# Kernel optimization log

Hardware: AMD Instinct MI355X
Metric: run time of the kernel (lower is better)

## Reference

```python
import jax, jax.numpy as jnp
import numpy as np

_K = 256  # d_model // 8


def setup_inputs() -> dict:
    key = jax.random.key(0)
    ks = jax.random.split(key, 7)
    B, T, D = 4, 4096, 2048
    x = jax.random.normal(ks[0], (B, T, D), jnp.float32)
    ema_mean = 0.1 * jax.random.normal(ks[1], (D,), jnp.float32)
    # ensure positive variance: ema_sq - ema_mean^2 in [0.5, 1.5]
    ema_sq = ema_mean ** 2 + 0.5 + jax.random.uniform(ks[2], (D,), jnp.float32)
    ema_out = jax.random.normal(ks[3], (D,), jnp.float32)
    log_tau = 0.1 * jax.random.normal(ks[4], (), jnp.float32)
    log_sigma_raw = 0.1 * jax.random.normal(ks[5], (), jnp.float32)
    log_w_raw = 0.1 * jax.random.normal(ks[6], (), jnp.float32)
    return {
        "x": x,
        "ema_mean": ema_mean,
        "ema_sq": ema_sq,
        "ema_out": ema_out,
        "log_tau": log_tau,
        "log_sigma_raw": log_sigma_raw,
        "log_w_raw": log_w_raw,
    }


def reference(x, ema_mean, ema_sq, ema_out, log_tau, log_sigma_raw, log_w_raw):
    tau = jnp.exp(log_tau)
    sigma = jax.nn.softplus(log_sigma_raw) + 0.01
    w = jax.nn.softplus(log_w_raw)

    out = jax.nn.gelu(x, approximate=False)  # F.gelu default = exact erf

    # z-score against EMA stats
    std = jnp.sqrt(jnp.clip(ema_sq - ema_mean ** 2, 1e-6, None))
    z = (x - ema_mean) / std

    # topk |z| over channel dim, gather z, mean of |z_topk|
    _, idx = jax.lax.top_k(jnp.abs(z), _K)          # idx: [B,T,K]
    z_topk = jnp.take_along_axis(z, idx, axis=-1)
    topk_mean = jnp.mean(jnp.abs(z_topk), axis=-1, keepdims=True)  # [B,T,1]
    surp = jnp.tanh(sigma * topk_mean)

    # cosine similarity of gelu output against EMA output direction
    ema_u = ema_out / (jnp.linalg.norm(ema_out) + 1e-8)
    out_n = out / jnp.maximum(
        jnp.linalg.norm(out, axis=-1, keepdims=True), 1e-12
    )  # F.normalize eps
    cos_out = jnp.sum(out_n * ema_u, axis=-1, keepdims=True)  # [B,T,1]

    gate = jnp.exp(-tau * cos_out) * (1.0 + w * surp)
    return out * gate
```

## Files before the change

kernel.cpp:

```cpp
#include <hip/hip_runtime.h>
#include <math.h>

#define D      2048
#define KSEL   256
#define NT     256
#define NBINS  512
#define ROWS   2

typedef float f4 __attribute__((ext_vector_type(4)));
typedef int   i4 __attribute__((ext_vector_type(4)));

__device__ __forceinline__ float fast_gelu(float x) {
    float x2 = x * x;
    float t  = fmaf(x2, -0.0713548162f, -1.5957691216f);
    float e  = __expf(x * t);
    return x * __builtin_amdgcn_rcpf(1.0f + e);
}

template<int CTRL, int RMASK>
__device__ __forceinline__ float dpp_mov_f(float v) {
    int r = __builtin_amdgcn_update_dpp(0, __builtin_bit_cast(int, v),
                                        CTRL, RMASK, 0xf, true);
    return __builtin_bit_cast(float, r);
}
template<int CTRL, int RMASK>
__device__ __forceinline__ int dpp_mov_i(int v) {
    return __builtin_amdgcn_update_dpp(0, v, CTRL, RMASK, 0xf, true);
}
__device__ __forceinline__ float wave_scan_f(float x) {
    x += dpp_mov_f<0x111, 0xf>(x);
    x += dpp_mov_f<0x112, 0xf>(x);
    x += dpp_mov_f<0x114, 0xf>(x);
    x += dpp_mov_f<0x118, 0xf>(x);
    x += dpp_mov_f<0x142, 0xa>(x);
    x += dpp_mov_f<0x143, 0xc>(x);
    return x;
}
__device__ __forceinline__ int wave_scan_i(int x) {
    x += dpp_mov_i<0x111, 0xf>(x);
    x += dpp_mov_i<0x112, 0xf>(x);
    x += dpp_mov_i<0x114, 0xf>(x);
    x += dpp_mov_i<0x118, 0xf>(x);
    x += dpp_mov_i<0x142, 0xa>(x);
    x += dpp_mov_i<0x143, 0xc>(x);
    return x;
}

__global__ __launch_bounds__(NT) void prep_kernel(
    const float* __restrict__ ema_mean,
    const float* __restrict__ ema_sq,
    const float* __restrict__ ema_out,
    const float* __restrict__ p_log_tau,
    const float* __restrict__ p_log_sigma,
    const float* __restrict__ p_log_w,
    float* __restrict__ ws)
{
    __shared__ float red[4];
    const int tid = threadIdx.x;
    float ss = 0.f;
#pragma unroll
    for (int k = 0; k < D / NT; ++k) {
        int i = tid + k * NT;
        float m = ema_mean[i];
        float v = fmaxf(fmaf(-m, m, ema_sq[i]), 1e-6f);
        float inv = 64.0f * __builtin_amdgcn_rsqf(v);
        ws[i]     = inv;
        ws[D + i] = -m * inv;
        float e = ema_out[i];
        ss = fmaf(e, e, ss);
    }
    ss = wave_scan_f(ss);
    if ((tid & 63) == 63) red[tid >> 6] = ss;
    __syncthreads();
    float inv_nrm = 1.0f / (sqrtf(red[0] + red[1] + red[2] + red[3]) + 1e-8f);
#pragma unroll
    for (int k = 0; k < D / NT; ++k) {
        int i = tid + k * NT;
        ws[2 * D + i] = ema_out[i] * inv_nrm;
    }
    if (tid == 0) {
        ws[3 * D + 0] = __expf(p_log_tau[0]);
        ws[3 * D + 1] = __logf(1.0f + __expf(p_log_sigma[0])) + 0.01f;
        ws[3 * D + 2] = __logf(1.0f + __expf(p_log_w[0]));
    }
}

__global__ __launch_bounds__(NT) void row_kernel(
    const float* __restrict__ x,
    const float* __restrict__ ws,
    float* __restrict__ out)
{
    __shared__ int   hist[NBINS];
    __shared__ float red[4][3];
    __shared__ int   bsel_sh, krem_sh;

    const int t    = threadIdx.x;
    const int wave = t >> 6;
    const int lane = t & 63;

    const float tau   = ws[3 * D + 0];
    const float sigma = ws[3 * D + 1];
    const float w     = ws[3 * D + 2];

    f4 aa = ((const f4*)ws)[t];
    f4 ab = ((const f4*)ws)[t + NT];
    f4 ba = ((const f4*)(ws + D))[t];
    f4 bb = ((const f4*)(ws + D))[t + NT];
    f4 ua = ((const f4*)(ws + 2 * D))[t];
    f4 ub = ((const f4*)(ws + 2 * D))[t + NT];
    const float a_[8] = {aa.x,aa.y,aa.z,aa.w, ab.x,ab.y,ab.z,ab.w};
    const float b_[8] = {ba.x,ba.y,ba.z,ba.w, bb.x,bb.y,bb.z,bb.w};
    const float u_[8] = {ua.x,ua.y,ua.z,ua.w, ub.x,ub.y,ub.z,ub.w};

    const size_t row0 = (size_t)blockIdx.x * ROWS;
    f4 xa = ((const f4*)(x + row0 * D))[t];
    f4 xb = ((const f4*)(x + row0 * D))[t + NT];

    hist[t] = 0;
    hist[t + NT] = 0;
    __syncthreads();

#pragma unroll
    for (int r = 0; r < ROWS; ++r) {
        const float xv[8] = {xa.x,xa.y,xa.z,xa.w, xb.x,xb.y,xb.z,xb.w};

        float g[8], av[8];
        float dot = 0.f, nrm = 0.f;
#pragma unroll
        for (int j = 0; j < 8; ++j) {
            float gg = fast_gelu(xv[j]);
            g[j] = gg;
            av[j] = fabsf(fmaf(xv[j], a_[j], b_[j]));
            dot = fmaf(gg, u_[j], dot);
            nrm = fmaf(gg, gg, nrm);
        }

        if (r + 1 < ROWS) {
            const float* xn = x + (row0 + r + 1) * D;
            xa = ((const f4*)xn)[t];
            xb = ((const f4*)xn)[t + NT];
        }

#pragma unroll
        for (int j = 0; j < 8; ++j) {
            int bin = (int)av[j];
            bin = bin > NBINS - 1 ? NBINS - 1 : bin;
            atomicAdd(&hist[(NBINS - 1) - bin], 1);
        }
        __syncthreads();

        if (wave == 0) {
            i4 va = *(const i4*)&hist[8 * lane];
            i4 vb = *(const i4*)&hist[8 * lane + 4];
            int c0 = va.x;
            int c1 = c0 + va.y;
            int c2 = c1 + va.z;
            int c3 = c2 + va.w;
            int c4 = c3 + vb.x;
            int c5 = c4 + vb.y;
            int c6 = c5 + vb.z;
            int c7 = c6 + vb.w;
            int incl = wave_scan_i(c7);
            int excl = incl - c7;
            int pre[8] = {0, c0, c1, c2, c3, c4, c5, c6};
            int cum[8] = {c0, c1, c2, c3, c4, c5, c6, c7};
#pragma unroll
            for (int k = 0; k < 8; ++k) {
                int s = excl + pre[k];
                int e = excl + cum[k];
                if (s < KSEL && e >= KSEL) {
                    bsel_sh = (NBINS - 1) - (8 * lane + k);
                    krem_sh = KSEL - s;
                }
            }
        }
        __syncthreads();

        const int   bsel = bsel_sh;
        const int   krem = krem_sh;
        const float hi  = (bsel == NBINS - 1) ? __builtin_inff() : (float)(bsel + 1);
        const float mid = (float)bsel + 0.5f;

        float s = 0.f;
#pragma unroll
        for (int j = 0; j < 8; ++j) {
            s += (av[j] >= hi) ? av[j] : 0.f;
        }

        dot = wave_scan_f(dot);
        nrm = wave_scan_f(nrm);
        s   = wave_scan_f(s);
        if (lane == 63) {
            red[wave][0] = dot; red[wave][1] = nrm; red[wave][2] = s;
        }
        hist[t] = 0;
        hist[t + NT] = 0;
        __syncthreads();

        dot = red[0][0] + red[1][0] + red[2][0] + red[3][0];
        nrm = red[0][1] + red[1][1] + red[2][1] + red[3][1];
        s   = red[0][2] + red[1][2] + red[2][2] + red[3][2];

        const float topk_mean = (s + (float)krem * mid) * (1.0f / (64.0f * KSEL));
        const float cosv = dot * __builtin_amdgcn_rsqf(fmaxf(nrm, 1e-24f));
        const float yt = sigma * topk_mean;
        const float et = __expf(-2.0f * yt);
        const float th = (1.0f - et) * __builtin_amdgcn_rcpf(1.0f + et);
        const float gate = __expf(-tau * cosv) * fmaf(w, th, 1.0f);

        f4 oa, ob;
        oa.x = g[0]*gate; oa.y = g[1]*gate; oa.z = g[2]*gate; oa.w = g[3]*gate;
        ob.x = g[4]*gate; ob.y = g[5]*gate; ob.z = g[6]*gate; ob.w = g[7]*gate;
        f4* outr = (f4*)(out + (row0 + r) * D);
        __builtin_nontemporal_store(oa, outr + t);
        __builtin_nontemporal_store(ob, outr + t + NT);
    }
}

extern "C" void kernel_launch(void* const* d_in, const int* in_sizes, int n_in,
                              void* d_out, int out_size, void* d_ws, size_t ws_size,
                              hipStream_t stream) {
    (void)n_in; (void)out_size; (void)ws_size;
    const float* x         = (const float*)d_in[0];
    const float* ema_mean  = (const float*)d_in[1];
    const float* ema_sq    = (const float*)d_in[2];
    const float* ema_out   = (const float*)d_in[3];
    const float* log_tau   = (const float*)d_in[4];
    const float* log_sigma = (const float*)d_in[5];
    const float* log_w     = (const float*)d_in[6];
    float* out = (float*)d_out;
    float* ws  = (float*)d_ws;

    prep_kernel<<<1, NT, 0, stream>>>(ema_mean, ema_sq, ema_out,
                                      log_tau, log_sigma, log_w, ws);
    const int rows = in_sizes[0] / D;
    row_kernel<<<rows / ROWS, NT, 0, stream>>>(x, ws, out);
}
```

Before: 50.20 us.

## Assign one row per wave with private histograms and fp16-packed register storage

The row kernel now maps one row to each wavefront instead of one row to the whole block. Each wave keeps its own LDS histogram and does its reductions with DPP scans plus readlane, so the block-wide __syncthreads barriers and the shared reduction buffers go away. To hold a whole row per lane (32 values), the GELU outputs and |z| values are stored packed as fp16, which reduces register pressure. The cost is lower precision: outputs are rounded through fp16 and top-k sums use fp16 |z| values. Each wave also reloads the EMA coefficient vectors itself, and the fp16 output error may exceed tolerance.

```diff
diff --git a/kernel.cpp b/kernel.cpp
--- a/kernel.cpp
+++ b/kernel.cpp
@@ -5,10 +5,11 @@
 #define KSEL   256
 #define NT     256
 #define NBINS  512
-#define ROWS   2
-
-typedef float f4 __attribute__((ext_vector_type(4)));
-typedef int   i4 __attribute__((ext_vector_type(4)));
+#define WPB    4
+
+typedef float  f4 __attribute__((ext_vector_type(4)));
+typedef int    i4 __attribute__((ext_vector_type(4)));
+typedef __fp16 h2 __attribute__((ext_vector_type(2)));
 
 __device__ __forceinline__ float fast_gelu(float x) {
     float x2 = x * x;
@@ -44,6 +45,20 @@
     x += dpp_mov_i<0x142, 0xa>(x);
     x += dpp_mov_i<0x143, 0xc>(x);
     return x;
+}
+__device__ __forceinline__ int wave_or_i(int x) {
+    x |= dpp_mov_i<0x111, 0xf>(x);
+    x |= dpp_mov_i<0x112, 0xf>(x);
+    x |= dpp_mov_i<0x114, 0xf>(x);
+    x |= dpp_mov_i<0x118, 0xf>(x);
+    x |= dpp_mov_i<0x142, 0xa>(x);
+    x |= dpp_mov_i<0x143, 0xc>(x);
+    return x;
+}
+__device__ __forceinline__ float wave_total_f(float x) {
+    float s = wave_scan_f(x);
+    int r = __builtin_amdgcn_readlane(__builtin_bit_cast(int, s), 63);
+    return __builtin_bit_cast(float, r);
 }
 
 __global__ __launch_bounds__(NT) void prep_kernel(
@@ -90,130 +105,129 @@
     const float* __restrict__ ws,
     float* __restrict__ out)
 {
-    __shared__ int   hist[NBINS];
-    __shared__ float red[4][3];
-    __shared__ int   bsel_sh, krem_sh;
+    __shared__ int hist[WPB * NBINS];
 
     const int t    = threadIdx.x;
-    const int wave = t >> 6;
+    const int wid  = t >> 6;
     const int lane = t & 63;
+    int* __restrict__ h = &hist[wid * NBINS];
+
+    *(i4*)&h[8 * lane]     = (i4)0;
+    *(i4*)&h[8 * lane + 4] = (i4)0;
 
     const float tau   = ws[3 * D + 0];
     const float sigma = ws[3 * D + 1];
     const float w     = ws[3 * D + 2];
 
-    f4 aa = ((const f4*)ws)[t];
-    f4 ab = ((const f4*)ws)[t + NT];
-    f4 ba = ((const f4*)(ws + D))[t];
-    f4 bb = ((const f4*)(ws + D))[t + NT];
-    f4 ua = ((const f4*)(ws + 2 * D))[t];
-    f4 ub = ((const f4*)(ws + 2 * D))[t + NT];
-    const float a_[8] = {aa.x,aa.y,aa.z,aa.w, ab.x,ab.y,ab.z,ab.w};
-    const float b_[8] = {ba.x,ba.y,ba.z,ba.w, bb.x,bb.y,bb.z,bb.w};
-    const float u_[8] = {ua.x,ua.y,ua.z,ua.w, ub.x,ub.y,ub.z,ub.w};
-
-    const size_t row0 = (size_t)blockIdx.x * ROWS;
-    f4 xa = ((const f4*)(x + row0 * D))[t];
-    f4 xb = ((const f4*)(x + row0 * D))[t + NT];
-
-    hist[t] = 0;
-    hist[t + NT] = 0;
-    __syncthreads();
-
-#pragma unroll
-    for (int r = 0; r < ROWS; ++r) {
-        const float xv[8] = {xa.x,xa.y,xa.z,xa.w, xb.x,xb.y,xb.z,xb.w};
-
-        float g[8], av[8];
-        float dot = 0.f, nrm = 0.f;
+    const size_t row = (size_t)blockIdx.x * WPB + wid;
+    const float* __restrict__ xr = x + row * D;
+
+    h2 gp[16];
+    h2 avp[16];
+    float dot = 0.f, nrm = 0.f;
+
+#pragma unroll
+    for (int c = 0; c < 4; ++c) {
+        const int vi = c * 128 + 2 * lane;
+        f4 x0 = ((const f4*)xr)[vi];
+        f4 x1 = ((const f4*)xr)[vi + 1];
+        f4 a0 = ((const f4*)ws)[vi];
+        f4 a1 = ((const f4*)ws)[vi + 1];
+        f4 b0 = ((const f4*)(ws + D))[vi];
+        f4 b1 = ((const f4*)(ws + D))[vi + 1];
+        f4 u0 = ((const f4*)(ws + 2 * D))[vi];
+        f4 u1 = ((const f4*)(ws + 2 * D))[vi + 1];
+
+        const float xv[8] = {x0.x,x0.y,x0.z,x0.w, x1.x,x1.y,x1.z,x1.w};
+        const float va[8] = {a0.x,a0.y,a0.z,a0.w, a1.x,a1.y,a1.z,a1.w};
+        const float vb[8] = {b0.x,b0.y,b0.z,b0.w, b1.x,b1.y,b1.z,b1.w};
+        const float vu[8] = {u0.x,u0.y,u0.z,u0.w, u1.x,u1.y,u1.z,u1.w};
+
+        float gg[8], av[8];
 #pragma unroll
         for (int j = 0; j < 8; ++j) {
-            float gg = fast_gelu(xv[j]);
-            g[j] = gg;
-            av[j] = fabsf(fmaf(xv[j], a_[j], b_[j]));
-            dot = fmaf(gg, u_[j], dot);
-            nrm = fmaf(gg, gg, nrm);
-        }
-
-        if (r + 1 < ROWS) {
-            const float* xn = x + (row0 + r + 1) * D;
-            xa = ((const f4*)xn)[t];
-            xb = ((const f4*)xn)[t + NT];
-        }
-
-#pragma unroll
-        for (int j = 0; j < 8; ++j) {
+            gg[j] = fast_gelu(xv[j]);
+            av[j] = fabsf(fmaf(xv[j], va[j], vb[j]));
+            dot = fmaf(gg[j], vu[j], dot);
+            nrm = fmaf(gg[j], gg[j], nrm);
             int bin = (int)av[j];
             bin = bin > NBINS - 1 ? NBINS - 1 : bin;
-            atomicAdd(&hist[(NBINS - 1) - bin], 1);
+            atomicAdd(&h[(NBINS - 1) - bin], 1);
         }
-        __syncthreads();
-
-        if (wave == 0) {
-            i4 va = *(const i4*)&hist[8 * lane];
-            i4 vb = *(const i4*)&hist[8 * lane + 4];
-            int c0 = va.x;
-            int c1 = c0 + va.y;
-            int c2 = c1 + va.z;
-            int c3 = c2 + va.w;
-            int c4 = c3 + vb.x;
-            int c5 = c4 + vb.y;
-            int c6 = c5 + vb.z;
-            int c7 = c6 + vb.w;
-            int incl = wave_scan_i(c7);
-            int excl = incl - c7;
-            int pre[8] = {0, c0, c1, c2, c3, c4, c5, c6};
-            int cum[8] = {c0, c1, c2, c3, c4, c5, c6, c7};
-#pragma unroll
-            for (int k = 0; k < 8; ++k) {
-                int s = excl + pre[k];
-                int e = excl + cum[k];
-                if (s < KSEL && e >= KSEL) {
-                    bsel_sh = (NBINS - 1) - (8 * lane + k);
-                    krem_sh = KSEL - s;
-                }
-            }
+#pragma unroll
+        for (int p = 0; p < 4; ++p) {
+            gp[c * 4 + p]  = __builtin_amdgcn_cvt_pkrtz(gg[2*p], gg[2*p+1]);
+            avp[c * 4 + p] = __builtin_amdgcn_cvt_pkrtz(av[2*p], av[2*p+1]);
         }
-        __syncthreads();
-
-        const int   bsel = bsel_sh;
-        const int   krem = krem_sh;
-        const float hi  = (bsel == NBINS - 1) ? __builtin_inff() : (float)(bsel + 1);
-        const float mid = (float)bsel + 0.5f;
-
-        float s = 0.f;
-#pragma unroll
-        for (int j = 0; j < 8; ++j) {
-            s += (av[j] >= hi) ? av[j] : 0.f;
+    }
+
+    i4 vA = *(const i4*)&h[8 * lane];
+    i4 vB = *(const i4*)&h[8 * lane + 4];
+    int c0 = vA.x;
+    int c1 = c0 + vA.y;
+    int c2 = c1 + vA.z;
+    int c3 = c2 + vA.w;
+    int c4 = c3 + vB.x;
+    int c5 = c4 + vB.y;
+    int c6 = c5 + vB.z;
+    int c7 = c6 + vB.w;
+    int incl = wave_scan_i(c7);
+    int excl = incl - c7;
+    {
+        const int pre[8] = {0, c0, c1, c2, c3, c4, c5, c6};
+        const int cum[8] = {c0, c1, c2, c3, c4, c5, c6, c7};
+        int enc = 0;
+#pragma unroll
+        for (int k = 0; k < 8; ++k) {
+            int s0 = excl + pre[k];
+            int e0 = excl + cum[k];
+            if (s0 < KSEL && e0 >= KSEL)
+                enc = ((NBINS - 1) - (8 * lane + k)) | ((KSEL - s0) << 16);
         }
-
-        dot = wave_scan_f(dot);
-        nrm = wave_scan_f(nrm);
-        s   = wave_scan_f(s);
-        if (lane == 63) {
-            red[wave][0] = dot; red[wave][1] = nrm; red[wave][2] = s;
-        }
-        hist[t] = 0;
-        hist[t + NT] = 0;
-        __syncthreads();
-
-        dot = red[0][0] + red[1][0] + red[2][0] + red[3][0];
-        nrm = red[0][1] + red[1][1] + red[2][1] + red[3][1];
-        s   = red[0][2] + red[1][2] + red[2][2] + red[3][2];
-
-        const float topk_mean = (s + (float)krem * mid) * (1.0f / (64.0f * KSEL));
-        const float cosv = dot * __builtin_amdgcn_rsqf(fmaxf(nrm, 1e-24f));
-        const float yt = sigma * topk_mean;
-        const float et = __expf(-2.0f * yt);
-        const float th = (1.0f - et) * __builtin_amdgcn_rcpf(1.0f + et);
-        const float gate = __expf(-tau * cosv) * fmaf(w, th, 1.0f);
-
-        f4 oa, ob;
-        oa.x = g[0]*gate; oa.y = g[1]*gate; oa.z = g[2]*gate; oa.w = g[3]*gate;
-        ob.x = g[4]*gate; ob.y = g[5]*gate; ob.z = g[6]*gate; ob.w = g[7]*gate;
-        f4* outr = (f4*)(out + (row0 + r) * D);
-        __builtin_nontemporal_store(oa, outr + t);
-        __builtin_nontemporal_store(ob, outr + t + NT);
+        enc = wave_or_i(enc);
+        enc = __builtin_amdgcn_readlane(enc, 63);
+        excl = enc;
+    }
+    const int   bsel = excl & 0xffff;
+    const int   krem = excl >> 16;
+    const float thr = (bsel == NBINS - 1) ? __builtin_inff() : (float)(bsel + 1);
+    const float mid = (float)bsel + 0.5f;
+
+    float s = 0.f;
+#pragma unroll
+    for (int i = 0; i < 16; ++i) {
+        float lo = (float)avp[i].x;
+        float hv = (float)avp[i].y;
+        s += (lo >= thr) ? lo : 0.f;
+        s += (hv >= thr) ? hv : 0.f;
+    }
+
+    dot = wave_total_f(dot);
+    nrm = wave_total_f(nrm);
+    s   = wave_total_f(s);
+
+    const float topk_mean = (s + (float)krem * mid) * (1.0f / (64.0f * KSEL));
+    const float cosv = dot * __builtin_amdgcn_rsqf(fmaxf(nrm, 1e-24f));
+    const float yt = sigma * topk_mean;
+    const float et = __expf(-2.0f * yt);
+    const float th = (1.0f - et) * __builtin_amdgcn_rcpf(1.0f + et);
+    const float gate = __expf(-tau * cosv) * fmaf(w, th, 1.0f);
+
+    f4* __restrict__ outr = (f4*)(out + row * D);
+#pragma unroll
+    for (int c = 0; c < 4; ++c) {
+        f4 o0, o1;
+        o0.x = (float)gp[c*4+0].x * gate;
+        o0.y = (float)gp[c*4+0].y * gate;
+        o0.z = (float)gp[c*4+1].x * gate;
+        o0.w = (float)gp[c*4+1].y * gate;
+        o1.x = (float)gp[c*4+2].x * gate;
+        o1.y = (float)gp[c*4+2].y * gate;
+        o1.z = (float)gp[c*4+3].x * gate;
+        o1.w = (float)gp[c*4+3].y * gate;
+        const int vi = c * 128 + 2 * lane;
+        __builtin_nontemporal_store(o0, outr + vi);
+        __builtin_nontemporal_store(o1, outr + vi + 1);
     }
 }
 
@@ -234,5 +248,5 @@
     prep_kernel<<<1, NT, 0, stream>>>(ema_mean, ema_sq, ema_out,
                                       log_tau, log_sigma, log_w, ws);
     const int rows = in_sizes[0] / D;
-    row_kernel<<<rows / ROWS, NT, 0, stream>>>(x, ws, out);
-}
+    row_kernel<<<rows / WPB, NT, 0, stream>>>(x, ws, out);
+}
```

Result: slower. 52.85 us (+5.3%).
